# Kernel optimization log

Measured on AMD Instinct MI355X. Metric: run time of the kernel, lower is better.

The kernel has to match this reference:

```python
import jax, jax.numpy as jnp
import numpy as np

IGNORE_THRESH = 0.5
OBJ_SCALE = 5.0
NOOBJ_SCALE = 1.0
XYWH_SCALE = 1.0
CLASS_SCALE = 1.0
GRID_SCALE = 1.0
ANCHOR_VALS = [10., 13., 16., 30., 33., 23., 30., 61., 62., 45., 59., 119., 116., 90., 156., 198., 373., 326.]


def setup_inputs() -> dict:
    key = jax.random.key(0)
    k1, k2, k3 = jax.random.split(key, 3)
    B, H, W, A, C, T, NET = 32, 32, 32, 9, 80, 50, 512
    y_pred = jax.random.normal(k1, (B, H, W, A * (5 + C)), jnp.float32) * 0.5
    y_true = jax.random.uniform(k2, (B, H, W, A, 5 + C), dtype=jnp.float32)
    true_boxes = jax.random.uniform(k3, (B, 1, 1, 1, T, 4), dtype=jnp.float32) * 10.0
    input_image = jnp.zeros((B, NET, NET, 3), jnp.float32)
    anchors = jnp.array(ANCHOR_VALS, jnp.float32).reshape(1, 1, 1, 9, 2)
    return {"input_image": input_image, "y_pred": y_pred, "y_true": y_true,
            "true_boxes": true_boxes, "anchors": anchors}


def reference(input_image, y_pred, y_true, true_boxes, anchors):
    B, H, W, A = y_true.shape[:4]
    y_pred = y_pred.reshape(B, H, W, A, -1)
    object_mask = y_true[..., 4:5]                                   # [B,H,W,9,1]
    grid_factor = jnp.array([W, H], jnp.float32).reshape(1, 1, 1, 1, 2)
    net_h, net_w = input_image.shape[1], input_image.shape[2]
    net_factor = jnp.array([net_w, net_h], jnp.float32).reshape(1, 1, 1, 1, 2)

    cx = jnp.broadcast_to(jnp.arange(W, dtype=jnp.float32).reshape(1, 1, W, 1, 1), (1, H, W, 1, 1))
    cy = jnp.broadcast_to(jnp.arange(H, dtype=jnp.float32).reshape(1, H, 1, 1, 1), (1, H, W, 1, 1))
    cell_grid = jnp.concatenate([cx, cy], -1)                        # [1,H,W,1,2]

    # adjust prediction
    pred_box_xy = cell_grid + jax.nn.sigmoid(y_pred[..., :2])
    pred_box_wh = y_pred[..., 2:4]
    pred_box_conf = jax.nn.sigmoid(y_pred[..., 4:5])
    pred_box_class = y_pred[..., 5:]

    # adjust ground truth
    true_box_xy = y_true[..., 0:2]
    true_box_wh = y_true[..., 2:4]
    true_box_conf = y_true[..., 4:5]
    true_box_class = jnp.argmax(y_true[..., 5:], -1)

    # pairwise IoU of every predicted box vs all true boxes
    t_xy = true_boxes[..., 0:2] / grid_factor                        # [B,1,1,1,T,2]
    t_wh = true_boxes[..., 2:4] / net_factor
    t_min = t_xy - t_wh / 2.0
    t_max = t_xy + t_wh / 2.0
    p_xy = (pred_box_xy / grid_factor)[..., None, :]                 # [B,H,W,9,1,2]
    p_wh = (jnp.exp(pred_box_wh) * anchors / net_factor)[..., None, :]
    p_min = p_xy - p_wh / 2.0
    p_max = p_xy + p_wh / 2.0
    iwh = jnp.maximum(jnp.minimum(p_max, t_max) - jnp.maximum(p_min, t_min), 0.0)
    inter = iwh[..., 0] * iwh[..., 1]                                # [B,H,W,9,T]
    union = p_wh[..., 0] * p_wh[..., 1] + t_wh[..., 0] * t_wh[..., 1] - inter
    best_ious = jnp.max(inter / union, axis=4)                       # [B,H,W,9]
    conf_delta = pred_box_conf * (best_ious < IGNORE_THRESH).astype(jnp.float32)[..., None]

    # warmup_batches = 0 -> non-warmup branch of tf.cond
    xywh_mask = object_mask

    wh_scale = jnp.exp(true_box_wh) * anchors / net_factor
    wh_scale = (2.0 - wh_scale[..., 0] * wh_scale[..., 1])[..., None]

    xy_delta = xywh_mask * (pred_box_xy - true_box_xy) * wh_scale * XYWH_SCALE
    wh_delta = xywh_mask * (pred_box_wh - true_box_wh) * wh_scale * XYWH_SCALE
    conf_delta = (object_mask * (pred_box_conf - true_box_conf) * OBJ_SCALE
                  + (1.0 - object_mask) * conf_delta * NOOBJ_SCALE)
    ce = -jnp.take_along_axis(jax.nn.log_softmax(pred_box_class, axis=-1),
                              true_box_class[..., None], axis=-1)    # [B,H,W,9,1]
    class_delta = object_mask * ce * CLASS_SCALE

    red = lambda t: jnp.sum(t, axis=(1, 2, 3, 4))
    loss = (red(jnp.square(xy_delta)) + red(jnp.square(wh_delta))
            + red(jnp.square(conf_delta)) + red(class_delta))
    return loss * GRID_SCALE
```

## Files before the change

kernel.cpp:

```cpp
#include <hip/hip_runtime.h>


constexpr int NT = 50;
typedef __attribute__((ext_vector_type(4))) float f4;

__global__ __launch_bounds__(256) void yolo_loss_kernel(
    const float* __restrict__ y_pred,
    const float* __restrict__ y_true,
    const float* __restrict__ true_boxes,
    const float* __restrict__ anchors,
    float* __restrict__ ws)
{
    __shared__ f4    s_box[4][NT];
    __shared__ float s_area[4][NT];
    __shared__ float s_anch[4][18];

    const int tid  = threadIdx.x;
    const int lane = tid & 63;
    const int wid  = tid >> 6;

    const int cell0 = blockIdx.x * 64;
    const int b     = cell0 / 9216;

    const int s  = tid & 3;
    const int g  = tid >> 2;
    const int gb = lane & ~3;

    const int cell  = cell0 + g;
    const int local = cell - b * 9216;
    const int a = local % 9;
    const int w = (local / 9) % 32;
    const int h = local / 288;

    const size_t base = (size_t)cell * 85 + s;
    const float* P = y_pred + base;
    const float* T = y_true + base;

    float pv[21], tv[21];
    #pragma unroll
    for (int j = 0; j < 21; ++j) pv[j] = P[4 * j];
    #pragma unroll
    for (int j = 0; j < 21; ++j) tv[j] = T[4 * j];
    float p84 = 0.0f, t84 = 0.0f;
    if (s == 0) { p84 = P[84]; t84 = T[84]; }

    if (lane < NT) {
        f4 tb;
        __builtin_memcpy(&tb, true_boxes + ((size_t)b * NT + lane) * 4, 16);
        const float tx = tb[0] * (1.0f / 32.0f);
        const float ty = tb[1] * (1.0f / 32.0f);
        const float tw = tb[2] * (1.0f / 512.0f);
        const float th = tb[3] * (1.0f / 512.0f);
        f4 e;
        e[0] = tx - tw * 0.5f;  e[1] = tx + tw * 0.5f;
        e[2] = ty - th * 0.5f;  e[3] = ty + th * 0.5f;
        s_box[wid][lane]  = e;
        s_area[wid][lane] = tw * th;
    }
    if (lane < 18) s_anch[wid][lane] = anchors[lane];

    asm volatile("s_waitcnt lgkmcnt(0)" ::: "memory");
    __builtin_amdgcn_sched_barrier(0);

    const float p0 = __shfl(pv[0], gb + 0);
    const float p1 = __shfl(pv[0], gb + 1);
    const float p2 = __shfl(pv[0], gb + 2);
    const float p3 = __shfl(pv[0], gb + 3);
    const float p4 = __shfl(pv[1], gb + 0);
    const float t0 = __shfl(tv[0], gb + 0);
    const float t1 = __shfl(tv[0], gb + 1);
    const float t2 = __shfl(tv[0], gb + 2);
    const float t3 = __shfl(tv[0], gb + 3);
    const float t4 = __shfl(tv[1], gb + 0);

    const float aw = s_anch[wid][a * 2 + 0];
    const float ah = s_anch[wid][a * 2 + 1];

    const float sig0  = 1.0f / (1.0f + __expf(-p0));
    const float sig1  = 1.0f / (1.0f + __expf(-p1));
    const float predx = (float)w + sig0;
    const float predy = (float)h + sig1;
    const float pconf = 1.0f / (1.0f + __expf(-p4));

    const float px = predx * (1.0f / 32.0f);
    const float py = predy * (1.0f / 32.0f);
    const float pw = __expf(p2) * aw * (1.0f / 512.0f);
    const float ph = __expf(p3) * ah * (1.0f / 512.0f);
    const float pminx = px - pw * 0.5f, pmaxx = px + pw * 0.5f;
    const float pminy = py - ph * 0.5f, pmaxy = py + ph * 0.5f;
    const float parea = pw * ph;

    int ig = 0;
    #pragma unroll
    for (int i = 0; i < 13; ++i) {
        const int box = i * 4 + s;
        if (box < NT) {
            const f4 e = s_box[wid][box];
            float iw = fminf(pmaxx, e[1]) - fmaxf(pminx, e[0]);
            float ih = fminf(pmaxy, e[3]) - fmaxf(pminy, e[2]);
            iw = fmaxf(iw, 0.0f);
            ih = fmaxf(ih, 0.0f);
            const float inter = iw * ih;
            const float uni   = parea + s_area[wid][box] - inter;
            ig |= (2.0f * inter >= uni) ? 1 : 0;
        }
    }
    ig |= __shfl_xor(ig, 1);
    ig |= __shfl_xor(ig, 2);

    float tmax = -1e30f, p_at = 0.0f, pmax = -1e30f;
    #pragma unroll
    for (int j = 0; j < 21; ++j) {
        const bool cls = (j >= 2) || (j == 1 && s != 0) || (4 * j + s >= 5);
        const float tcm = cls ? tv[j] : -1e30f;
        const float pcm = cls ? pv[j] : -1e30f;
        if (tcm > tmax) { tmax = tcm; p_at = pv[j]; }
        pmax = fmaxf(pmax, pcm);
    }
    {
        const float tcm = (s == 0) ? t84 : -1e30f;
        if (tcm > tmax) { tmax = tcm; p_at = p84; }
        pmax = fmaxf(pmax, (s == 0) ? p84 : -1e30f);
    }
    #pragma unroll
    for (int d = 1; d <= 2; d <<= 1) {
        const float ot = __shfl_xor(tmax, d);
        const float op = __shfl_xor(p_at, d);
        if (ot > tmax) { tmax = ot; p_at = op; }
        pmax = fmaxf(pmax, __shfl_xor(pmax, d));
    }

    float acc[4] = {0.0f, 0.0f, 0.0f, 0.0f};
    #pragma unroll
    for (int j = 0; j < 21; ++j) {
        const bool cls = (j >= 2) || (j == 1 && s != 0) || (4 * j + s >= 5);
        const float e = __expf(pv[j] - pmax);
        acc[j & 3] += cls ? e : 0.0f;
    }
    {
        const float e = __expf(p84 - pmax);
        acc[1] += (s == 0) ? e : 0.0f;
    }
    float sum = (acc[0] + acc[1]) + (acc[2] + acc[3]);
    sum += __shfl_xor(sum, 1);
    sum += __shfl_xor(sum, 2);
    const float ce = (pmax + __logf(sum)) - p_at;

    const float om  = t4;
    const float ew  = __expf(t2) * aw * (1.0f / 512.0f);
    const float eh  = __expf(t3) * ah * (1.0f / 512.0f);
    const float whs = 2.0f - ew * eh;

    const float xyd0 = om * (predx - t0) * whs;
    const float xyd1 = om * (predy - t1) * whs;
    const float whd0 = om * (p2 - t2) * whs;
    const float whd1 = om * (p3 - t3) * whs;
    const float cd   = om * (pconf - t4) * 5.0f + (1.0f - om) * (ig ? 0.0f : pconf);

    float partial = xyd0 * xyd0 + xyd1 * xyd1 + whd0 * whd0 + whd1 * whd1 +
                    cd * cd + om * ce;
    partial = (s == 0) ? partial : 0.0f;

    #pragma unroll
    for (int off = 32; off > 0; off >>= 1)
        partial += __shfl_down(partial, off);
    if (lane == 0)
        ws[blockIdx.x * 4 + wid] = partial;
}

__global__ __launch_bounds__(64) void yolo_reduce_kernel(
    const float* __restrict__ ws,
    float* __restrict__ out)
{
    const int b    = blockIdx.x;
    const int lane = threadIdx.x;
    const float* p = ws + b * 576;

    float v = 0.0f;
    #pragma unroll
    for (int k = 0; k < 9; ++k) v += p[lane + 64 * k];
    #pragma unroll
    for (int off = 32; off > 0; off >>= 1)
        v += __shfl_down(v, off);
    if (lane == 0) out[b] = v;
}

extern "C" void kernel_launch(void* const* d_in, const int* in_sizes, int n_in,
                              void* d_out, int out_size, void* d_ws, size_t ws_size,
                              hipStream_t stream) {
    const float* y_pred     = (const float*)d_in[1];
    const float* y_true     = (const float*)d_in[2];
    const float* true_boxes = (const float*)d_in[3];
    const float* anchors    = (const float*)d_in[4];
    float* out = (float*)d_out;
    float* ws  = (float*)d_ws;

    dim3 grid(294912 / 64);
    yolo_loss_kernel<<<grid, 256, 0, stream>>>(y_pred, y_true, true_boxes, anchors, ws);
    yolo_reduce_kernel<<<32, 64, 0, stream>>>(ws, out);
}
```

Baseline: 38.43 us.

## Process four cell groups per block with double-buffered register prefetch

Each block now covers 256 cells instead of 64, so the grid is four times smaller. Each wave loops over four 64-cell chunks, loading the next chunk's y_pred/y_true into a second register set while computing the current one. The true-box and anchor setup in shared memory is paid once per four chunks, and the reduce kernel reads fewer partials. The cost is roughly double the register footprint, which lowers occupancy and leaves fewer blocks to spread across CUs.

```diff
diff --git a/kernel.cpp b/kernel.cpp
--- a/kernel.cpp
+++ b/kernel.cpp
@@ -18,31 +18,30 @@
     const int tid  = threadIdx.x;
     const int lane = tid & 63;
     const int wid  = tid >> 6;
-
-    const int cell0 = blockIdx.x * 64;
-    const int b     = cell0 / 9216;
-
-    const int s  = tid & 3;
-    const int g  = tid >> 2;
-    const int gb = lane & ~3;
-
-    const int cell  = cell0 + g;
-    const int local = cell - b * 9216;
-    const int a = local % 9;
-    const int w = (local / 9) % 32;
-    const int h = local / 288;
-
-    const size_t base = (size_t)cell * 85 + s;
-    const float* P = y_pred + base;
-    const float* T = y_true + base;
-
-    float pv[21], tv[21];
-    #pragma unroll
-    for (int j = 0; j < 21; ++j) pv[j] = P[4 * j];
-    #pragma unroll
-    for (int j = 0; j < 21; ++j) tv[j] = T[4 * j];
-    float p84 = 0.0f, t84 = 0.0f;
-    if (s == 0) { p84 = P[84]; t84 = T[84]; }
+    const int s    = tid & 3;
+    const int g    = tid >> 2;
+    const int gb   = lane & ~3;
+
+    const int cellB = blockIdx.x * 256;
+    const int b     = cellB / 9216;
+
+    auto loadC = [&](int K, float (&PV)[21], float (&TV)[21],
+                     float& P84, float& T84) {
+        const size_t base_ = (size_t)(cellB + K * 64 + g) * 85 + s;
+        const float* P_ = y_pred + base_;
+        const float* T_ = y_true + base_;
+        #pragma unroll
+        for (int j = 0; j < 21; ++j) PV[j] = P_[4 * j];
+        #pragma unroll
+        for (int j = 0; j < 21; ++j) TV[j] = T_[4 * j];
+        P84 = 0.0f; T84 = 0.0f;
+        if (s == 0) { P84 = P_[84]; T84 = T_[84]; }
+    };
+
+    float pvA[21], tvA[21], p84A, t84A;
+    float pvB[21], tvB[21], p84B, t84B;
+
+    loadC(0, pvA, tvA, p84A, t84A);
 
     if (lane < NT) {
         f4 tb;
@@ -58,114 +57,136 @@
         s_area[wid][lane] = tw * th;
     }
     if (lane < 18) s_anch[wid][lane] = anchors[lane];
-
     asm volatile("s_waitcnt lgkmcnt(0)" ::: "memory");
     __builtin_amdgcn_sched_barrier(0);
 
-    const float p0 = __shfl(pv[0], gb + 0);
-    const float p1 = __shfl(pv[0], gb + 1);
-    const float p2 = __shfl(pv[0], gb + 2);
-    const float p3 = __shfl(pv[0], gb + 3);
-    const float p4 = __shfl(pv[1], gb + 0);
-    const float t0 = __shfl(tv[0], gb + 0);
-    const float t1 = __shfl(tv[0], gb + 1);
-    const float t2 = __shfl(tv[0], gb + 2);
-    const float t3 = __shfl(tv[0], gb + 3);
-    const float t4 = __shfl(tv[1], gb + 0);
-
-    const float aw = s_anch[wid][a * 2 + 0];
-    const float ah = s_anch[wid][a * 2 + 1];
-
-    const float sig0  = 1.0f / (1.0f + __expf(-p0));
-    const float sig1  = 1.0f / (1.0f + __expf(-p1));
-    const float predx = (float)w + sig0;
-    const float predy = (float)h + sig1;
-    const float pconf = 1.0f / (1.0f + __expf(-p4));
-
-    const float px = predx * (1.0f / 32.0f);
-    const float py = predy * (1.0f / 32.0f);
-    const float pw = __expf(p2) * aw * (1.0f / 512.0f);
-    const float ph = __expf(p3) * ah * (1.0f / 512.0f);
-    const float pminx = px - pw * 0.5f, pmaxx = px + pw * 0.5f;
-    const float pminy = py - ph * 0.5f, pmaxy = py + ph * 0.5f;
-    const float parea = pw * ph;
-
-    int ig = 0;
-    #pragma unroll
-    for (int i = 0; i < 13; ++i) {
-        const int box = i * 4 + s;
-        if (box < NT) {
-            const f4 e = s_box[wid][box];
-            float iw = fminf(pmaxx, e[1]) - fmaxf(pminx, e[0]);
-            float ih = fminf(pmaxy, e[3]) - fmaxf(pminy, e[2]);
-            iw = fmaxf(iw, 0.0f);
-            ih = fmaxf(ih, 0.0f);
-            const float inter = iw * ih;
-            const float uni   = parea + s_area[wid][box] - inter;
-            ig |= (2.0f * inter >= uni) ? 1 : 0;
-        }
-    }
-    ig |= __shfl_xor(ig, 1);
-    ig |= __shfl_xor(ig, 2);
-
-    float tmax = -1e30f, p_at = 0.0f, pmax = -1e30f;
-    #pragma unroll
-    for (int j = 0; j < 21; ++j) {
-        const bool cls = (j >= 2) || (j == 1 && s != 0) || (4 * j + s >= 5);
-        const float tcm = cls ? tv[j] : -1e30f;
-        const float pcm = cls ? pv[j] : -1e30f;
-        if (tcm > tmax) { tmax = tcm; p_at = pv[j]; }
-        pmax = fmaxf(pmax, pcm);
-    }
-    {
-        const float tcm = (s == 0) ? t84 : -1e30f;
-        if (tcm > tmax) { tmax = tcm; p_at = p84; }
-        pmax = fmaxf(pmax, (s == 0) ? p84 : -1e30f);
-    }
-    #pragma unroll
-    for (int d = 1; d <= 2; d <<= 1) {
-        const float ot = __shfl_xor(tmax, d);
-        const float op = __shfl_xor(p_at, d);
-        if (ot > tmax) { tmax = ot; p_at = op; }
-        pmax = fmaxf(pmax, __shfl_xor(pmax, d));
-    }
-
-    float acc[4] = {0.0f, 0.0f, 0.0f, 0.0f};
-    #pragma unroll
-    for (int j = 0; j < 21; ++j) {
-        const bool cls = (j >= 2) || (j == 1 && s != 0) || (4 * j + s >= 5);
-        const float e = __expf(pv[j] - pmax);
-        acc[j & 3] += cls ? e : 0.0f;
-    }
-    {
-        const float e = __expf(p84 - pmax);
-        acc[1] += (s == 0) ? e : 0.0f;
-    }
-    float sum = (acc[0] + acc[1]) + (acc[2] + acc[3]);
-    sum += __shfl_xor(sum, 1);
-    sum += __shfl_xor(sum, 2);
-    const float ce = (pmax + __logf(sum)) - p_at;
-
-    const float om  = t4;
-    const float ew  = __expf(t2) * aw * (1.0f / 512.0f);
-    const float eh  = __expf(t3) * ah * (1.0f / 512.0f);
-    const float whs = 2.0f - ew * eh;
-
-    const float xyd0 = om * (predx - t0) * whs;
-    const float xyd1 = om * (predy - t1) * whs;
-    const float whd0 = om * (p2 - t2) * whs;
-    const float whd1 = om * (p3 - t3) * whs;
-    const float cd   = om * (pconf - t4) * 5.0f + (1.0f - om) * (ig ? 0.0f : pconf);
-
-    float partial = xyd0 * xyd0 + xyd1 * xyd1 + whd0 * whd0 + whd1 * whd1 +
-                    cd * cd + om * ce;
-    partial = (s == 0) ? partial : 0.0f;
+    auto doCell = [&](int K, const float (&pv)[21], const float (&tv)[21],
+                      float p84, float t84) -> float {
+        const int cell  = cellB + K * 64 + g;
+        const int local = cell - b * 9216;
+        const int a = local % 9;
+        const int w = (local / 9) % 32;
+        const int h = local / 288;
+
+        const float p0 = __shfl(pv[0], gb + 0);
+        const float p1 = __shfl(pv[0], gb + 1);
+        const float p2 = __shfl(pv[0], gb + 2);
+        const float p3 = __shfl(pv[0], gb + 3);
+        const float p4 = __shfl(pv[1], gb + 0);
+        const float t0 = __shfl(tv[0], gb + 0);
+        const float t1 = __shfl(tv[0], gb + 1);
+        const float t2 = __shfl(tv[0], gb + 2);
+        const float t3 = __shfl(tv[0], gb + 3);
+        const float t4 = __shfl(tv[1], gb + 0);
+
+        const float aw = s_anch[wid][a * 2 + 0];
+        const float ah = s_anch[wid][a * 2 + 1];
+
+        const float sig0  = 1.0f / (1.0f + __expf(-p0));
+        const float sig1  = 1.0f / (1.0f + __expf(-p1));
+        const float predx = (float)w + sig0;
+        const float predy = (float)h + sig1;
+        const float pconf = 1.0f / (1.0f + __expf(-p4));
+
+        const float px = predx * (1.0f / 32.0f);
+        const float py = predy * (1.0f / 32.0f);
+        const float pw = __expf(p2) * aw * (1.0f / 512.0f);
+        const float ph = __expf(p3) * ah * (1.0f / 512.0f);
+        const float pminx = px - pw * 0.5f, pmaxx = px + pw * 0.5f;
+        const float pminy = py - ph * 0.5f, pmaxy = py + ph * 0.5f;
+        const float parea = pw * ph;
+
+        int ig = 0;
+        #pragma unroll
+        for (int i = 0; i < 13; ++i) {
+            const int box = i * 4 + s;
+            if (box < NT) {
+                const f4 e = s_box[wid][box];
+                float iw = fminf(pmaxx, e[1]) - fmaxf(pminx, e[0]);
+                float ih = fminf(pmaxy, e[3]) - fmaxf(pminy, e[2]);
+                iw = fmaxf(iw, 0.0f);
+                ih = fmaxf(ih, 0.0f);
+                const float inter = iw * ih;
+                const float uni   = parea + s_area[wid][box] - inter;
+                ig |= (2.0f * inter >= uni) ? 1 : 0;
+            }
+        }
+        ig |= __shfl_xor(ig, 1);
+        ig |= __shfl_xor(ig, 2);
+
+        float tmax = -1e30f, p_at = 0.0f, pmax = -1e30f;
+        #pragma unroll
+        for (int j = 0; j < 21; ++j) {
+            const bool cls = (j >= 2) || (j == 1 && s != 0) || (4 * j + s >= 5);
+            const float tcm = cls ? tv[j] : -1e30f;
+            const float pcm = cls ? pv[j] : -1e30f;
+            if (tcm > tmax) { tmax = tcm; p_at = pv[j]; }
+            pmax = fmaxf(pmax, pcm);
+        }
+        {
+            const float tcm = (s == 0) ? t84 : -1e30f;
+            if (tcm > tmax) { tmax = tcm; p_at = p84; }
+            pmax = fmaxf(pmax, (s == 0) ? p84 : -1e30f);
+        }
+        #pragma unroll
+        for (int d = 1; d <= 2; d <<= 1) {
+            const float ot = __shfl_xor(tmax, d);
+            const float op = __shfl_xor(p_at, d);
+            if (ot > tmax) { tmax = ot; p_at = op; }
+            pmax = fmaxf(pmax, __shfl_xor(pmax, d));
+        }
+
+        float acc0 = 0.f, acc1 = 0.f, acc2 = 0.f, acc3 = 0.f;
+        #pragma unroll
+        for (int j = 0; j < 21; ++j) {
+            const bool cls = (j >= 2) || (j == 1 && s != 0) || (4 * j + s >= 5);
+            const float e = __expf(pv[j] - pmax);
+            const float v = cls ? e : 0.0f;
+            if ((j & 3) == 0) acc0 += v;
+            else if ((j & 3) == 1) acc1 += v;
+            else if ((j & 3) == 2) acc2 += v;
+            else acc3 += v;
+        }
+        {
+            const float e = __expf(p84 - pmax);
+            acc1 += (s == 0) ? e : 0.0f;
+        }
+        float sum = (acc0 + acc1) + (acc2 + acc3);
+        sum += __shfl_xor(sum, 1);
+        sum += __shfl_xor(sum, 2);
+        const float ce = (pmax + __logf(sum)) - p_at;
+
+        const float om  = t4;
+        const float ew  = __expf(t2) * aw * (1.0f / 512.0f);
+        const float eh  = __expf(t3) * ah * (1.0f / 512.0f);
+        const float whs = 2.0f - ew * eh;
+
+        const float xyd0 = om * (predx - t0) * whs;
+        const float xyd1 = om * (predy - t1) * whs;
+        const float whd0 = om * (p2 - t2) * whs;
+        const float whd1 = om * (p3 - t3) * whs;
+        const float cd   = om * (pconf - t4) * 5.0f +
+                           (1.0f - om) * (ig ? 0.0f : pconf);
+
+        const float partial = xyd0 * xyd0 + xyd1 * xyd1 + whd0 * whd0 +
+                              whd1 * whd1 + cd * cd + om * ce;
+        return (s == 0) ? partial : 0.0f;
+    };
+
+    float accp = 0.0f;
+    loadC(1, pvB, tvB, p84B, t84B);
+    accp += doCell(0, pvA, tvA, p84A, t84A);
+    loadC(2, pvA, tvA, p84A, t84A);
+    accp += doCell(1, pvB, tvB, p84B, t84B);
+    loadC(3, pvB, tvB, p84B, t84B);
+    accp += doCell(2, pvA, tvA, p84A, t84A);
+    accp += doCell(3, pvB, tvB, p84B, t84B);
 
     #pragma unroll
     for (int off = 32; off > 0; off >>= 1)
-        partial += __shfl_down(partial, off);
+        accp += __shfl_down(accp, off);
     if (lane == 0)
-        ws[blockIdx.x * 4 + wid] = partial;
+        ws[blockIdx.x * 4 + wid] = accp;
 }
 
 __global__ __launch_bounds__(64) void yolo_reduce_kernel(
@@ -174,11 +195,9 @@
 {
     const int b    = blockIdx.x;
     const int lane = threadIdx.x;
-    const float* p = ws + b * 576;
-
-    float v = 0.0f;
-    #pragma unroll
-    for (int k = 0; k < 9; ++k) v += p[lane + 64 * k];
+    const float* p = ws + b * 144;
+
+    float v = p[lane] + p[lane + 64] + ((lane < 16) ? p[lane + 128] : 0.0f);
     #pragma unroll
     for (int off = 32; off > 0; off >>= 1)
         v += __shfl_down(v, off);
@@ -195,7 +214,7 @@
     float* out = (float*)d_out;
     float* ws  = (float*)d_ws;
 
-    dim3 grid(294912 / 64);
+    dim3 grid(294912 / 256);
     yolo_loss_kernel<<<grid, 256, 0, stream>>>(y_pred, y_true, true_boxes, anchors, ws);
     yolo_reduce_kernel<<<32, 64, 0, stream>>>(ws, out);
 }
```

Result: slower. 46.95 us (+22.2%).
